# Optimization experiments

Measured on AMD Instinct MI355X. Metric: run time of the kernel, lower is better.

The kernel has to match this reference:

```python
import jax, jax.numpy as jnp
import numpy as np

B, NF, E, A = 4096, 40, 64, 32  # batch, num feature fields, embedding_size, attention_size


def setup_inputs() -> dict:
    key = jax.random.key(0)
    kx, kw, kb, kh = jax.random.split(key, 4)
    return {
        "x": jax.random.normal(kx, (B, NF, E), dtype=jnp.float32),
        "W": jax.random.normal(kw, (E, A), dtype=jnp.float32) * 0.05,  # random_normal init
        "b": jax.random.normal(kb, (A,), dtype=jnp.float32) * 0.05,
        "h": jax.random.normal(kh, (A,), dtype=jnp.float32) * 0.05,
        "p": jnp.ones((E, 1), dtype=jnp.float32),  # 'ones' initializer
    }


def reference(x, W, b, h, p):
    nf = x.shape[1]
    # pairwise (i<j) element-wise products, same ordering as the double loop
    ii, jj = np.triu_indices(nf, k=1)
    ewp = x[:, ii, :] * x[:, jj, :]                      # (B, P, E), P = nf*(nf-1)/2
    # attention MLP: relu(ewp @ W + b) . h, then exp-normalize over pairs
    a = jax.nn.relu(jnp.einsum('bpe,ea->bpa', ewp, W) + b)  # (B, P, A)
    e = jnp.exp(jnp.sum(a * h, axis=-1))                 # (B, P)  (faithful: no max-subtract)
    att = e / jnp.sum(e, axis=1, keepdims=True)          # (B, P)
    pooled = jnp.einsum('bp,bpe->be', att, ewp)          # attention-weighted sum over pairs
    return pooled @ p                                    # (B, 1)
```

## Files before the change

kernel.cpp:

```cpp
#include <hip/hip_runtime.h>

#define NFEAT 40
#define EMB   64
#define ATT   32
#define NPAIR 780
#define NTILE 49
#define XH_S  72
#define XREG  (NFEAT * XH_S)

typedef __attribute__((ext_vector_type(8))) _Float16 f16x8;
typedef __attribute__((ext_vector_type(4))) _Float16 f16x4;
typedef __attribute__((ext_vector_type(4))) float    f32x4;
typedef __attribute__((ext_vector_type(2))) unsigned u32x2;

template <int CTRL>
__device__ __forceinline__ float dpp_add_f(float v) {
  int t = __builtin_amdgcn_update_dpp(0, __float_as_int(v), CTRL, 0xF, 0xF, true);
  return v + __int_as_float(t);
}
__device__ __forceinline__ float rowsum16(float v) {
  v = dpp_add_f<0x128>(v);
  v = dpp_add_f<0x124>(v);
  v = dpp_add_f<0x122>(v);
  v = dpp_add_f<0x121>(v);
  return v;
}

__device__ __forceinline__ float xgroup_sum(float v) {
#if __has_builtin(__builtin_amdgcn_permlane16_swap) && __has_builtin(__builtin_amdgcn_permlane32_swap)
  {
    auto a = __builtin_amdgcn_permlane16_swap(__float_as_uint(v), __float_as_uint(v), false, false);
    v = __uint_as_float(a[0]) + __uint_as_float(a[1]);
    auto b = __builtin_amdgcn_permlane32_swap(__float_as_uint(v), __float_as_uint(v), false, false);
    v = __uint_as_float(b[0]) + __uint_as_float(b[1]);
  }
#else
  v += __shfl_xor(v, 16, 64);
  v += __shfl_xor(v, 32, 64);
#endif
  return v;
}

__device__ __forceinline__ int pair_off(int i) { return 39 * i - (i * (i - 1)) / 2; }

extern "C" __global__ __launch_bounds__(256)
void afm_kernel(const float* __restrict__ xg, const float* __restrict__ Wg,
                const float* __restrict__ bg, const float* __restrict__ hg,
                const float* __restrict__ pg, float* __restrict__ outg, int nbatch) {
  __shared__ __align__(16) _Float16 xh[2 * XREG];
  __shared__ unsigned prtp[25 * 32];
  __shared__ float red[4][2];

  const int tid  = threadIdx.x;
  const int lane = tid & 63, wid = tid >> 6;
  const int l15  = lane & 15, hk = lane >> 4;
  const int half = wid & 1;
  const int breg = wid >> 1;
  const int bb   = blockIdx.x * 2 + breg;
  const bool live = bb < nbatch;

  for (int p = tid; p < NTILE * 16; p += 256) {
    int i = 0, j = 0;
    if (p < NPAIR) {
      i = (int)((79.0f - sqrtf(6241.0f - 8.0f * (float)p)) * 0.5f);
      if (i < 0) i = 0;
      while (pair_off(i + 1) <= p) ++i;
      while (pair_off(i) > p) --i;
      j = i + 1 + (p - pair_off(i));
    }
    int t = p >> 4, l = p & 15;
    prtp[(t >> 1) * 32 + l * 2 + (t & 1)] =
        (unsigned)(i * 144) | ((unsigned)(j * 144) << 16);
  }

  f16x8 wf0[2], wf1[2], wf2[2];
#pragma unroll
  for (int kk = 0; kk < 2; kk++) {
    f16x8 r0, r1, r2;
#pragma unroll
    for (int t = 0; t < 8; t++) {
      int krow = kk * 32 + hk * 8 + t;
      r0[t] = (_Float16)Wg[krow * ATT + l15];
      r1[t] = (_Float16)Wg[krow * ATT + 16 + l15];
      _Float16 pv = (_Float16)pg[krow];
      r2[t] = (l15 == 0) ? pv : (_Float16)0.f;
    }
    wf0[kk] = r0; wf1[kk] = r1; wf2[kk] = r2;
  }
  const float4 b0 = *(const float4*)&bg[hk * 4];
  const float4 b1 = *(const float4*)&bg[16 + hk * 4];
  const f32x4 cb0 = {b0.x, b0.y, b0.z, b0.w};
  const f32x4 cb1 = {b1.x, b1.y, b1.z, b1.w};
  const float L2E = 1.4426950408889634f;
  float4 h0 = *(const float4*)&hg[hk * 4];
  float4 h1 = *(const float4*)&hg[16 + hk * 4];
  h0.x *= L2E; h0.y *= L2E; h0.z *= L2E; h0.w *= L2E;
  h1.x *= L2E; h1.y *= L2E; h1.z *= L2E; h1.w *= L2E;
  const f32x4 kz = {0.f, 0.f, 0.f, 0.f};

  if (live) {
    const float4* xsrc = (const float4*)(xg + (size_t)bb * (NFEAT * EMB));
    _Float16* xw = &xh[breg * XREG];
#pragma unroll
    for (int f = lane + half * 64; f < NFEAT * EMB / 4; f += 128) {
      float4 v = xsrc[f];
      int row = f >> 4, c = (f & 15) * 4;
      f16x4 h4 = {(_Float16)v.x, (_Float16)v.y, (_Float16)v.z, (_Float16)v.w};
      *(f16x4*)&xw[row * XH_S + c] = h4;
    }
  }
  __syncthreads();

  float sum_e = 0.f, sum_es = 0.f;
  const unsigned wh = (unsigned)(breg * (XREG * 2) + hk * 16);

  auto tile = [&](unsigned pij, bool full) {
    const unsigned offi = (pij & 0xFFFFu) + wh;
    const unsigned offj = (pij >> 16) + wh;
    const f16x8 xi0 = *(const f16x8*)((const char*)xh + offi);
    const f16x8 xj0 = *(const f16x8*)((const char*)xh + offj);
    const f16x8 xi1 = *(const f16x8*)((const char*)xh + offi + 64);
    const f16x8 xj1 = *(const f16x8*)((const char*)xh + offj + 64);
    f16x8 af0 = xi0 * xj0;
    f16x8 af1 = xi1 * xj1;
    f32x4 acc0 = __builtin_amdgcn_mfma_f32_16x16x32_f16(wf0[0], af0, cb0, 0, 0, 0);
    f32x4 acc1 = __builtin_amdgcn_mfma_f32_16x16x32_f16(wf1[0], af0, cb1, 0, 0, 0);
    f32x4 acc2 = __builtin_amdgcn_mfma_f32_16x16x32_f16(wf2[0], af0, kz, 0, 0, 0);
    acc0 = __builtin_amdgcn_mfma_f32_16x16x32_f16(wf0[1], af1, acc0, 0, 0, 0);
    acc1 = __builtin_amdgcn_mfma_f32_16x16x32_f16(wf1[1], af1, acc1, 0, 0, 0);
    acc2 = __builtin_amdgcn_mfma_f32_16x16x32_f16(wf2[1], af1, acc2, 0, 0, 0);
    float va = fmaf(fmaxf(acc0[0], 0.f), h0.x,
               fmaf(fmaxf(acc0[1], 0.f), h0.y,
               fmaf(fmaxf(acc0[2], 0.f), h0.z,
                    fmaxf(acc0[3], 0.f) * h0.w)));
    float vb = fmaf(fmaxf(acc1[0], 0.f), h1.x,
               fmaf(fmaxf(acc1[1], 0.f), h1.y,
               fmaf(fmaxf(acc1[2], 0.f), h1.z,
                    fmaxf(acc1[3], 0.f) * h1.w)));
    float v = xgroup_sum(va + vb);
    float e = exp2f(v);
    if (!full) e = (l15 < 12) ? e : 0.f;
    sum_e += e;
    sum_es = fmaf(e, acc2[0], sum_es);
  };

  if (live) {
    const int k0 = half ? 12 : 0;
    const int k1 = half ? 24 : 12;
#pragma unroll 4
    for (int k = k0; k < k1; ++k) {
      u32x2 pp = *(const u32x2*)&prtp[k * 32 + l15 * 2];
      tile(pp[0], true);
      tile(pp[1], true);
    }
    if (!half) tile(prtp[24 * 32 + l15 * 2], false);

    sum_e  = rowsum16(sum_e);
    sum_es = rowsum16(sum_es);
    if (lane == 0) { red[wid][0] = sum_e; red[wid][1] = sum_es; }
  }
  __syncthreads();
  if (live && lane == 0 && half == 0) {
    float Z = red[wid][0] + red[wid + 1][0];
    float S = red[wid][1] + red[wid + 1][1];
    outg[bb] = S / Z;
  }
}

extern "C" void kernel_launch(void* const* d_in, const int* in_sizes, int n_in,
                              void* d_out, int out_size, void* d_ws, size_t ws_size,
                              hipStream_t stream) {
  const float* xg = (const float*)d_in[0];
  const float* Wg = (const float*)d_in[1];
  const float* bg = (const float*)d_in[2];
  const float* hg = (const float*)d_in[3];
  const float* pg = (const float*)d_in[4];
  float* outg = (float*)d_out;
  const int Bn = in_sizes[0] / (NFEAT * EMB);
  const int nblk = (Bn + 1) / 2;
  afm_kernel<<<dim3(nblk), dim3(256), 0, stream>>>(xg, Wg, bg, hg, pg, outg, Bn);
}
```

Measured before the change: 37.55 us.

## Assign one batch row per wave and software-pipeline pair tile loop

Each wave now handles a whole batch row instead of two waves splitting one row. Blocks cover four rows, which removes the cross-wave shared-memory reduction and the second barrier, and halves the number of blocks. The pair loop is restructured to issue all LDS loads for two tiles before the MFMAs, to prefetch the next pair-index word, and to use a shallower epilogue reduction tree. The cost is twice the LDS per block, which may lower occupancy, plus a longer serial chain per wave.

```diff
diff --git a/kernel.cpp b/kernel.cpp
--- a/kernel.cpp
+++ b/kernel.cpp
@@ -47,16 +47,13 @@
 void afm_kernel(const float* __restrict__ xg, const float* __restrict__ Wg,
                 const float* __restrict__ bg, const float* __restrict__ hg,
                 const float* __restrict__ pg, float* __restrict__ outg, int nbatch) {
-  __shared__ __align__(16) _Float16 xh[2 * XREG];
+  __shared__ __align__(16) _Float16 xh[4 * XREG];
   __shared__ unsigned prtp[25 * 32];
-  __shared__ float red[4][2];
 
   const int tid  = threadIdx.x;
   const int lane = tid & 63, wid = tid >> 6;
   const int l15  = lane & 15, hk = lane >> 4;
-  const int half = wid & 1;
-  const int breg = wid >> 1;
-  const int bb   = blockIdx.x * 2 + breg;
+  const int bb   = blockIdx.x * 4 + wid;
   const bool live = bb < nbatch;
 
   for (int p = tid; p < NTILE * 16; p += 256) {
@@ -98,11 +95,11 @@
   h1.x *= L2E; h1.y *= L2E; h1.z *= L2E; h1.w *= L2E;
   const f32x4 kz = {0.f, 0.f, 0.f, 0.f};
 
+  _Float16* xw = &xh[wid * XREG];
   if (live) {
     const float4* xsrc = (const float4*)(xg + (size_t)bb * (NFEAT * EMB));
-    _Float16* xw = &xh[breg * XREG];
 #pragma unroll
-    for (int f = lane + half * 64; f < NFEAT * EMB / 4; f += 128) {
+    for (int f = lane; f < NFEAT * EMB / 4; f += 64) {
       float4 v = xsrc[f];
       int row = f >> 4, c = (f & 15) * 4;
       f16x4 h4 = {(_Float16)v.x, (_Float16)v.y, (_Float16)v.z, (_Float16)v.w};
@@ -111,60 +108,77 @@
   }
   __syncthreads();
 
+  if (!live) return;
+  const unsigned wh = (unsigned)(wid * (XREG * 2) + hk * 16);
+
   float sum_e = 0.f, sum_es = 0.f;
-  const unsigned wh = (unsigned)(breg * (XREG * 2) + hk * 16);
 
-  auto tile = [&](unsigned pij, bool full) {
-    const unsigned offi = (pij & 0xFFFFu) + wh;
-    const unsigned offj = (pij >> 16) + wh;
-    const f16x8 xi0 = *(const f16x8*)((const char*)xh + offi);
-    const f16x8 xj0 = *(const f16x8*)((const char*)xh + offj);
-    const f16x8 xi1 = *(const f16x8*)((const char*)xh + offi + 64);
-    const f16x8 xj1 = *(const f16x8*)((const char*)xh + offj + 64);
-    f16x8 af0 = xi0 * xj0;
-    f16x8 af1 = xi1 * xj1;
-    f32x4 acc0 = __builtin_amdgcn_mfma_f32_16x16x32_f16(wf0[0], af0, cb0, 0, 0, 0);
-    f32x4 acc1 = __builtin_amdgcn_mfma_f32_16x16x32_f16(wf1[0], af0, cb1, 0, 0, 0);
-    f32x4 acc2 = __builtin_amdgcn_mfma_f32_16x16x32_f16(wf2[0], af0, kz, 0, 0, 0);
-    acc0 = __builtin_amdgcn_mfma_f32_16x16x32_f16(wf0[1], af1, acc0, 0, 0, 0);
-    acc1 = __builtin_amdgcn_mfma_f32_16x16x32_f16(wf1[1], af1, acc1, 0, 0, 0);
-    acc2 = __builtin_amdgcn_mfma_f32_16x16x32_f16(wf2[1], af1, acc2, 0, 0, 0);
-    float va = fmaf(fmaxf(acc0[0], 0.f), h0.x,
-               fmaf(fmaxf(acc0[1], 0.f), h0.y,
-               fmaf(fmaxf(acc0[2], 0.f), h0.z,
-                    fmaxf(acc0[3], 0.f) * h0.w)));
-    float vb = fmaf(fmaxf(acc1[0], 0.f), h1.x,
-               fmaf(fmaxf(acc1[1], 0.f), h1.y,
-               fmaf(fmaxf(acc1[2], 0.f), h1.z,
-                    fmaxf(acc1[3], 0.f) * h1.w)));
-    float v = xgroup_sum(va + vb);
+  auto epilogue = [&](const f32x4& a0, const f32x4& a1, const f32x4& a2, bool full) {
+    float t0 = fmaf(fmaxf(a0[0], 0.f), h0.x, fmaxf(a0[1], 0.f) * h0.y);
+    float t1 = fmaf(fmaxf(a0[2], 0.f), h0.z, fmaxf(a0[3], 0.f) * h0.w);
+    float t2 = fmaf(fmaxf(a1[0], 0.f), h1.x, fmaxf(a1[1], 0.f) * h1.y);
+    float t3 = fmaf(fmaxf(a1[2], 0.f), h1.z, fmaxf(a1[3], 0.f) * h1.w);
+    float v = xgroup_sum((t0 + t1) + (t2 + t3));
     float e = exp2f(v);
     if (!full) e = (l15 < 12) ? e : 0.f;
     sum_e += e;
-    sum_es = fmaf(e, acc2[0], sum_es);
+    sum_es = fmaf(e, a2[0], sum_es);
   };
 
-  if (live) {
-    const int k0 = half ? 12 : 0;
-    const int k1 = half ? 24 : 12;
-#pragma unroll 4
-    for (int k = k0; k < k1; ++k) {
-      u32x2 pp = *(const u32x2*)&prtp[k * 32 + l15 * 2];
-      tile(pp[0], true);
-      tile(pp[1], true);
-    }
-    if (!half) tile(prtp[24 * 32 + l15 * 2], false);
+  u32x2 pp = *(const u32x2*)&prtp[l15 * 2];
+#pragma unroll 2
+  for (int k = 0; k < 24; ++k) {
+    const unsigned oiA = (pp[0] & 0xFFFFu) + wh, ojA = (pp[0] >> 16) + wh;
+    const unsigned oiB = (pp[1] & 0xFFFFu) + wh, ojB = (pp[1] >> 16) + wh;
+    const f16x8 xiA0 = *(const f16x8*)((const char*)xh + oiA);
+    const f16x8 xjA0 = *(const f16x8*)((const char*)xh + ojA);
+    const f16x8 xiA1 = *(const f16x8*)((const char*)xh + oiA + 64);
+    const f16x8 xjA1 = *(const f16x8*)((const char*)xh + ojA + 64);
+    const f16x8 xiB0 = *(const f16x8*)((const char*)xh + oiB);
+    const f16x8 xjB0 = *(const f16x8*)((const char*)xh + ojB);
+    const f16x8 xiB1 = *(const f16x8*)((const char*)xh + oiB + 64);
+    const f16x8 xjB1 = *(const f16x8*)((const char*)xh + ojB + 64);
+    if (k < 23) pp = *(const u32x2*)&prtp[(k + 1) * 32 + l15 * 2];
+    f16x8 afA0 = xiA0 * xjA0;
+    f16x8 afA1 = xiA1 * xjA1;
+    f32x4 aA0 = __builtin_amdgcn_mfma_f32_16x16x32_f16(wf0[0], afA0, cb0, 0, 0, 0);
+    f32x4 aA1 = __builtin_amdgcn_mfma_f32_16x16x32_f16(wf1[0], afA0, cb1, 0, 0, 0);
+    f32x4 aA2 = __builtin_amdgcn_mfma_f32_16x16x32_f16(wf2[0], afA0, kz, 0, 0, 0);
+    aA0 = __builtin_amdgcn_mfma_f32_16x16x32_f16(wf0[1], afA1, aA0, 0, 0, 0);
+    aA1 = __builtin_amdgcn_mfma_f32_16x16x32_f16(wf1[1], afA1, aA1, 0, 0, 0);
+    aA2 = __builtin_amdgcn_mfma_f32_16x16x32_f16(wf2[1], afA1, aA2, 0, 0, 0);
+    f16x8 afB0 = xiB0 * xjB0;
+    f16x8 afB1 = xiB1 * xjB1;
+    f32x4 aB0 = __builtin_amdgcn_mfma_f32_16x16x32_f16(wf0[0], afB0, cb0, 0, 0, 0);
+    f32x4 aB1 = __builtin_amdgcn_mfma_f32_16x16x32_f16(wf1[0], afB0, cb1, 0, 0, 0);
+    f32x4 aB2 = __builtin_amdgcn_mfma_f32_16x16x32_f16(wf2[0], afB0, kz, 0, 0, 0);
+    aB0 = __builtin_amdgcn_mfma_f32_16x16x32_f16(wf0[1], afB1, aB0, 0, 0, 0);
+    aB1 = __builtin_amdgcn_mfma_f32_16x16x32_f16(wf1[1], afB1, aB1, 0, 0, 0);
+    aB2 = __builtin_amdgcn_mfma_f32_16x16x32_f16(wf2[1], afB1, aB2, 0, 0, 0);
+    epilogue(aA0, aA1, aA2, true);
+    epilogue(aB0, aB1, aB2, true);
+  }
+  {
+    const unsigned pij = prtp[24 * 32 + l15 * 2];
+    const unsigned oi = (pij & 0xFFFFu) + wh, oj = (pij >> 16) + wh;
+    const f16x8 xi0 = *(const f16x8*)((const char*)xh + oi);
+    const f16x8 xj0 = *(const f16x8*)((const char*)xh + oj);
+    const f16x8 xi1 = *(const f16x8*)((const char*)xh + oi + 64);
+    const f16x8 xj1 = *(const f16x8*)((const char*)xh + oj + 64);
+    f16x8 af0 = xi0 * xj0;
+    f16x8 af1 = xi1 * xj1;
+    f32x4 a0 = __builtin_amdgcn_mfma_f32_16x16x32_f16(wf0[0], af0, cb0, 0, 0, 0);
+    f32x4 a1 = __builtin_amdgcn_mfma_f32_16x16x32_f16(wf1[0], af0, cb1, 0, 0, 0);
+    f32x4 a2 = __builtin_amdgcn_mfma_f32_16x16x32_f16(wf2[0], af0, kz, 0, 0, 0);
+    a0 = __builtin_amdgcn_mfma_f32_16x16x32_f16(wf0[1], af1, a0, 0, 0, 0);
+    a1 = __builtin_amdgcn_mfma_f32_16x16x32_f16(wf1[1], af1, a1, 0, 0, 0);
+    a2 = __builtin_amdgcn_mfma_f32_16x16x32_f16(wf2[1], af1, a2, 0, 0, 0);
+    epilogue(a0, a1, a2, false);
+  }
 
-    sum_e  = rowsum16(sum_e);
-    sum_es = rowsum16(sum_es);
-    if (lane == 0) { red[wid][0] = sum_e; red[wid][1] = sum_es; }
-  }
-  __syncthreads();
-  if (live && lane == 0 && half == 0) {
-    float Z = red[wid][0] + red[wid + 1][0];
-    float S = red[wid][1] + red[wid + 1][1];
-    outg[bb] = S / Z;
-  }
+  sum_e  = rowsum16(sum_e);
+  sum_es = rowsum16(sum_es);
+  if (lane == 0) outg[bb] = sum_es / sum_e;
 }
 
 extern "C" void kernel_launch(void* const* d_in, const int* in_sizes, int n_in,
@@ -177,6 +191,6 @@
   const float* pg = (const float*)d_in[4];
   float* outg = (float*)d_out;
   const int Bn = in_sizes[0] / (NFEAT * EMB);
-  const int nblk = (Bn + 1) / 2;
+  const int nblk = (Bn + 3) / 4;
   afm_kernel<<<dim3(nblk), dim3(256), 0, stream>>>(xg, Wg, bg, hg, pg, outg, Bn);
 }
```

After: 38.95 us. +3.7%, slower.

## Split weight/pair-table prep into a pre-kernel and use one wave per batch row

Applied to the files above, without the earlier changes.

A small three-block pre-kernel builds the packed fp16 MFMA weight fragments, the pair offset table and the bias/h constants into the workspace once per call. The main kernel now runs one wave per batch row with 128-thread blocks, dropping the per-block pair-table computation, the scattered W gathers, the cross-wave reduction and both __syncthreads. Each wave then handles all 780 pairs itself and reads the pair table from global/L1 with a prefetch. The costs are a second kernel launch and fewer waves in total, so each wave's serial work doubles.

```diff
diff --git a/kernel.cpp b/kernel.cpp
--- a/kernel.cpp
+++ b/kernel.cpp
@@ -8,8 +8,11 @@
 #define XH_S  72
 #define XREG  (NFEAT * XH_S)
 
+#define WS_PRT   0
+#define WS_WF    1024
+#define WS_CONST 4096
+
 typedef __attribute__((ext_vector_type(8))) _Float16 f16x8;
-typedef __attribute__((ext_vector_type(4))) _Float16 f16x4;
 typedef __attribute__((ext_vector_type(4))) float    f32x4;
 typedef __attribute__((ext_vector_type(2))) unsigned u32x2;
 
@@ -25,7 +28,6 @@
   v = dpp_add_f<0x121>(v);
   return v;
 }
-
 __device__ __forceinline__ float xgroup_sum(float v) {
 #if __has_builtin(__builtin_amdgcn_permlane16_swap) && __has_builtin(__builtin_amdgcn_permlane32_swap)
   {
@@ -40,79 +42,107 @@
 #endif
   return v;
 }
-
 __device__ __forceinline__ int pair_off(int i) { return 39 * i - (i * (i - 1)) / 2; }
 
 extern "C" __global__ __launch_bounds__(256)
-void afm_kernel(const float* __restrict__ xg, const float* __restrict__ Wg,
-                const float* __restrict__ bg, const float* __restrict__ hg,
-                const float* __restrict__ pg, float* __restrict__ outg, int nbatch) {
+void afm_pre(const float* __restrict__ Wg, const float* __restrict__ bg,
+             const float* __restrict__ hg, const float* __restrict__ pg,
+             unsigned* __restrict__ ws) {
+  __shared__ float Wl[EMB * ATT];
+  const int tid = threadIdx.x;
+  const float L2E = 1.4426950408889634f;
+
+  if (blockIdx.x == 0) {
+    for (int f = tid; f < EMB * ATT / 4; f += 256)
+      *(float4*)&Wl[f * 4] = ((const float4*)Wg)[f];
+    __syncthreads();
+    for (int o = tid; o < 1536; o += 256) {
+      int lane = o / 24, rem = o % 24, frag = rem >> 2, pi = rem & 3;
+      int kk = frag / 3, which = frag % 3;
+      int l15 = lane & 15, hk = lane >> 4;
+      unsigned out = 0;
+#pragma unroll
+      for (int s = 0; s < 2; s++) {
+        int t = pi * 2 + s;
+        int krow = kk * 32 + hk * 8 + t;
+        float v = (which == 0) ? Wl[krow * ATT + l15]
+                : (which == 1) ? Wl[krow * ATT + 16 + l15]
+                               : ((l15 == 0) ? pg[krow] : 0.f);
+        _Float16 hv = (_Float16)v;
+        unsigned short bits = __builtin_bit_cast(unsigned short, hv);
+        out |= (unsigned)bits << (16 * s);
+      }
+      ws[WS_WF + lane * 24 + rem] = out;
+    }
+  } else if (blockIdx.x == 1) {
+    for (int p = tid; p < NTILE * 16; p += 256) {
+      int i = 0, j = 0;
+      if (p < NPAIR) {
+        i = (int)((79.0f - sqrtf(6241.0f - 8.0f * (float)p)) * 0.5f);
+        if (i < 0) i = 0;
+        while (pair_off(i + 1) <= p) ++i;
+        while (pair_off(i) > p) --i;
+        j = i + 1 + (p - pair_off(i));
+      }
+      int t = p >> 4, l = p & 15;
+      ws[WS_PRT + (t >> 1) * 32 + l * 2 + (t & 1)] =
+          (unsigned)(i * 144) | ((unsigned)(j * 144) << 16);
+    }
+  } else if (blockIdx.x == 2) {
+    for (int o = tid; o < 1024; o += 256) {
+      int lane = o >> 4, r = o & 15;
+      int hk = lane >> 4, g = r >> 2, e = r & 3;
+      float v;
+      if (g == 0)      v = bg[hk * 4 + e];
+      else if (g == 1) v = bg[16 + hk * 4 + e];
+      else if (g == 2) v = hg[hk * 4 + e] * L2E;
+      else             v = hg[16 + hk * 4 + e] * L2E;
+      ((float*)ws)[WS_CONST + o] = v;
+    }
+  }
+}
+
+extern "C" __global__ __launch_bounds__(128)
+void afm_kernel(const float* __restrict__ xg, const unsigned* __restrict__ ws,
+                float* __restrict__ outg, int nbatch) {
   __shared__ __align__(16) _Float16 xh[2 * XREG];
-  __shared__ unsigned prtp[25 * 32];
-  __shared__ float red[4][2];
-
-  const int tid  = threadIdx.x;
-  const int lane = tid & 63, wid = tid >> 6;
-  const int l15  = lane & 15, hk = lane >> 4;
-  const int half = wid & 1;
-  const int breg = wid >> 1;
-  const int bb   = blockIdx.x * 2 + breg;
-  const bool live = bb < nbatch;
-
-  for (int p = tid; p < NTILE * 16; p += 256) {
-    int i = 0, j = 0;
-    if (p < NPAIR) {
-      i = (int)((79.0f - sqrtf(6241.0f - 8.0f * (float)p)) * 0.5f);
-      if (i < 0) i = 0;
-      while (pair_off(i + 1) <= p) ++i;
-      while (pair_off(i) > p) --i;
-      j = i + 1 + (p - pair_off(i));
-    }
-    int t = p >> 4, l = p & 15;
-    prtp[(t >> 1) * 32 + l * 2 + (t & 1)] =
-        (unsigned)(i * 144) | ((unsigned)(j * 144) << 16);
-  }
-
+
+  const int lane = threadIdx.x & 63, wid = threadIdx.x >> 6;
+  const int l15 = lane & 15, hk = lane >> 4;
+  const int bb = blockIdx.x * 2 + wid;
+  if (bb >= nbatch) return;
+
+  union { uint4 u; f16x8 h; } cv;
+  const uint4* wfp = (const uint4*)(ws + WS_WF + lane * 24);
   f16x8 wf0[2], wf1[2], wf2[2];
+  cv.u = wfp[0]; wf0[0] = cv.h;
+  cv.u = wfp[1]; wf1[0] = cv.h;
+  cv.u = wfp[2]; wf2[0] = cv.h;
+  cv.u = wfp[3]; wf0[1] = cv.h;
+  cv.u = wfp[4]; wf1[1] = cv.h;
+  cv.u = wfp[5]; wf2[1] = cv.h;
+  const float4* cp = (const float4*)((const float*)ws + WS_CONST + lane * 16);
+  const float4 c0 = cp[0], c1 = cp[1];
+  const float4 h0 = cp[2], h1 = cp[3];
+  const f32x4 cb0 = {c0.x, c0.y, c0.z, c0.w};
+  const f32x4 cb1 = {c1.x, c1.y, c1.z, c1.w};
+  const f32x4 kz  = {0.f, 0.f, 0.f, 0.f};
+
+  _Float16* xw = &xh[wid * XREG];
+  const float* xsrc = xg + (size_t)bb * (NFEAT * EMB);
 #pragma unroll
-  for (int kk = 0; kk < 2; kk++) {
-    f16x8 r0, r1, r2;
-#pragma unroll
-    for (int t = 0; t < 8; t++) {
-      int krow = kk * 32 + hk * 8 + t;
-      r0[t] = (_Float16)Wg[krow * ATT + l15];
-      r1[t] = (_Float16)Wg[krow * ATT + 16 + l15];
-      _Float16 pv = (_Float16)pg[krow];
-      r2[t] = (l15 == 0) ? pv : (_Float16)0.f;
-    }
-    wf0[kk] = r0; wf1[kk] = r1; wf2[kk] = r2;
-  }
-  const float4 b0 = *(const float4*)&bg[hk * 4];
-  const float4 b1 = *(const float4*)&bg[16 + hk * 4];
-  const f32x4 cb0 = {b0.x, b0.y, b0.z, b0.w};
-  const f32x4 cb1 = {b1.x, b1.y, b1.z, b1.w};
-  const float L2E = 1.4426950408889634f;
-  float4 h0 = *(const float4*)&hg[hk * 4];
-  float4 h1 = *(const float4*)&hg[16 + hk * 4];
-  h0.x *= L2E; h0.y *= L2E; h0.z *= L2E; h0.w *= L2E;
-  h1.x *= L2E; h1.y *= L2E; h1.z *= L2E; h1.w *= L2E;
-  const f32x4 kz = {0.f, 0.f, 0.f, 0.f};
-
-  if (live) {
-    const float4* xsrc = (const float4*)(xg + (size_t)bb * (NFEAT * EMB));
-    _Float16* xw = &xh[breg * XREG];
-#pragma unroll
-    for (int f = lane + half * 64; f < NFEAT * EMB / 4; f += 128) {
-      float4 v = xsrc[f];
-      int row = f >> 4, c = (f & 15) * 4;
-      f16x4 h4 = {(_Float16)v.x, (_Float16)v.y, (_Float16)v.z, (_Float16)v.w};
-      *(f16x4*)&xw[row * XH_S + c] = h4;
-    }
-  }
-  __syncthreads();
-
+  for (int it = 0; it < 5; it++) {
+    int g0 = (it * 64 + lane) * 8;
+    float4 a = *(const float4*)&xsrc[g0];
+    float4 b = *(const float4*)&xsrc[g0 + 4];
+    int row = g0 >> 6, c = g0 & 63;
+    f16x8 v = {(_Float16)a.x, (_Float16)a.y, (_Float16)a.z, (_Float16)a.w,
+               (_Float16)b.x, (_Float16)b.y, (_Float16)b.z, (_Float16)b.w};
+    *(f16x8*)&xw[row * XH_S + c] = v;
+  }
+
+  const unsigned wh = (unsigned)(wid * (XREG * 2) + hk * 16);
   float sum_e = 0.f, sum_es = 0.f;
-  const unsigned wh = (unsigned)(breg * (XREG * 2) + hk * 16);
 
   auto tile = [&](unsigned pij, bool full) {
     const unsigned offi = (pij & 0xFFFFu) + wh;
@@ -123,48 +153,36 @@
     const f16x8 xj1 = *(const f16x8*)((const char*)xh + offj + 64);
     f16x8 af0 = xi0 * xj0;
     f16x8 af1 = xi1 * xj1;
-    f32x4 acc0 = __builtin_amdgcn_mfma_f32_16x16x32_f16(wf0[0], af0, cb0, 0, 0, 0);
-    f32x4 acc1 = __builtin_amdgcn_mfma_f32_16x16x32_f16(wf1[0], af0, cb1, 0, 0, 0);
-    f32x4 acc2 = __builtin_amdgcn_mfma_f32_16x16x32_f16(wf2[0], af0, kz, 0, 0, 0);
-    acc0 = __builtin_amdgcn_mfma_f32_16x16x32_f16(wf0[1], af1, acc0, 0, 0, 0);
-    acc1 = __builtin_amdgcn_mfma_f32_16x16x32_f16(wf1[1], af1, acc1, 0, 0, 0);
-    acc2 = __builtin_amdgcn_mfma_f32_16x16x32_f16(wf2[1], af1, acc2, 0, 0, 0);
-    float va = fmaf(fmaxf(acc0[0], 0.f), h0.x,
-               fmaf(fmaxf(acc0[1], 0.f), h0.y,
-               fmaf(fmaxf(acc0[2], 0.f), h0.z,
-                    fmaxf(acc0[3], 0.f) * h0.w)));
-    float vb = fmaf(fmaxf(acc1[0], 0.f), h1.x,
-               fmaf(fmaxf(acc1[1], 0.f), h1.y,
-               fmaf(fmaxf(acc1[2], 0.f), h1.z,
-                    fmaxf(acc1[3], 0.f) * h1.w)));
-    float v = xgroup_sum(va + vb);
+    f32x4 a0 = __builtin_amdgcn_mfma_f32_16x16x32_f16(wf0[0], af0, cb0, 0, 0, 0);
+    f32x4 a1 = __builtin_amdgcn_mfma_f32_16x16x32_f16(wf1[0], af0, cb1, 0, 0, 0);
+    f32x4 a2 = __builtin_amdgcn_mfma_f32_16x16x32_f16(wf2[0], af0, kz, 0, 0, 0);
+    a0 = __builtin_amdgcn_mfma_f32_16x16x32_f16(wf0[1], af1, a0, 0, 0, 0);
+    a1 = __builtin_amdgcn_mfma_f32_16x16x32_f16(wf1[1], af1, a1, 0, 0, 0);
+    a2 = __builtin_amdgcn_mfma_f32_16x16x32_f16(wf2[1], af1, a2, 0, 0, 0);
+    float t0 = fmaf(fmaxf(a0[0], 0.f), h0.x, fmaxf(a0[1], 0.f) * h0.y);
+    float t1 = fmaf(fmaxf(a0[2], 0.f), h0.z, fmaxf(a0[3], 0.f) * h0.w);
+    float t2 = fmaf(fmaxf(a1[0], 0.f), h1.x, fmaxf(a1[1], 0.f) * h1.y);
+    float t3 = fmaf(fmaxf(a1[2], 0.f), h1.z, fmaxf(a1[3], 0.f) * h1.w);
+    float v = xgroup_sum((t0 + t1) + (t2 + t3));
     float e = exp2f(v);
     if (!full) e = (l15 < 12) ? e : 0.f;
     sum_e += e;
-    sum_es = fmaf(e, acc2[0], sum_es);
+    sum_es = fmaf(e, a2[0], sum_es);
   };
 
-  if (live) {
-    const int k0 = half ? 12 : 0;
-    const int k1 = half ? 24 : 12;
+  u32x2 pp = *(const u32x2*)(ws + WS_PRT + l15 * 2);
 #pragma unroll 4
-    for (int k = k0; k < k1; ++k) {
-      u32x2 pp = *(const u32x2*)&prtp[k * 32 + l15 * 2];
-      tile(pp[0], true);
-      tile(pp[1], true);
-    }
-    if (!half) tile(prtp[24 * 32 + l15 * 2], false);
-
-    sum_e  = rowsum16(sum_e);
-    sum_es = rowsum16(sum_es);
-    if (lane == 0) { red[wid][0] = sum_e; red[wid][1] = sum_es; }
-  }
-  __syncthreads();
-  if (live && lane == 0 && half == 0) {
-    float Z = red[wid][0] + red[wid + 1][0];
-    float S = red[wid][1] + red[wid + 1][1];
-    outg[bb] = S / Z;
-  }
+  for (int k = 0; k < 24; ++k) {
+    const unsigned pij0 = pp[0], pij1 = pp[1];
+    if (k < 23) pp = *(const u32x2*)(ws + WS_PRT + (k + 1) * 32 + l15 * 2);
+    tile(pij0, true);
+    tile(pij1, true);
+  }
+  tile(ws[WS_PRT + 24 * 32 + l15 * 2], false);
+
+  sum_e  = rowsum16(sum_e);
+  sum_es = rowsum16(sum_es);
+  if (lane == 0) outg[bb] = sum_es / sum_e;
 }
 
 extern "C" void kernel_launch(void* const* d_in, const int* in_sizes, int n_in,
@@ -176,7 +194,8 @@
   const float* hg = (const float*)d_in[3];
   const float* pg = (const float*)d_in[4];
   float* outg = (float*)d_out;
+  unsigned* ws = (unsigned*)d_ws;
   const int Bn = in_sizes[0] / (NFEAT * EMB);
-  const int nblk = (Bn + 1) / 2;
-  afm_kernel<<<dim3(nblk), dim3(256), 0, stream>>>(xg, Wg, bg, hg, pg, outg, Bn);
-}
+  afm_pre<<<dim3(3), dim3(256), 0, stream>>>(Wg, bg, hg, pg, ws);
+  afm_kernel<<<dim3((Bn + 1) / 2), dim3(128), 0, stream>>>(xg, ws, outg, Bn);
+}
```

Measured after the change: 41.38 us. 1.1x slower.

## Assign two batch rows per wave and use packed fp16 dot for relu-h

Applied to the files above, without the earlier changes.

Restructures the work split so each wave processes two full batch rows (8 per block) instead of two waves sharing one row. This removes the cross-wave shared-memory reduction and second barrier, and interleaves independent MFMA chains for latency hiding. The relu·h step becomes packed fp16 convert, max and fdot2, and staging uses pkrtz conversion. Shared memory grows fourfold, which may reduce occupancy, and the fp16 rounding of activations before the h dot adds precision loss.

```diff
diff --git a/kernel.cpp b/kernel.cpp
--- a/kernel.cpp
+++ b/kernel.cpp
@@ -9,9 +9,9 @@
 #define XREG  (NFEAT * XH_S)
 
 typedef __attribute__((ext_vector_type(8))) _Float16 f16x8;
-typedef __attribute__((ext_vector_type(4))) _Float16 f16x4;
 typedef __attribute__((ext_vector_type(4))) float    f32x4;
 typedef __attribute__((ext_vector_type(2))) unsigned u32x2;
+typedef __attribute__((ext_vector_type(2))) __fp16   h2_t;
 
 template <int CTRL>
 __device__ __forceinline__ float dpp_add_f(float v) {
@@ -25,7 +25,6 @@
   v = dpp_add_f<0x121>(v);
   return v;
 }
-
 __device__ __forceinline__ float xgroup_sum(float v) {
 #if __has_builtin(__builtin_amdgcn_permlane16_swap) && __has_builtin(__builtin_amdgcn_permlane32_swap)
   {
@@ -40,24 +39,31 @@
 #endif
   return v;
 }
-
 __device__ __forceinline__ int pair_off(int i) { return 39 * i - (i * (i - 1)) / 2; }
+
+__device__ __forceinline__ float reludot2(float s0, float s1, h2_t h2, float c) {
+  h2_t r = __builtin_amdgcn_cvt_pkrtz(s0, s1);
+  r = __builtin_elementwise_max(r, h2_t{(__fp16)0.f, (__fp16)0.f});
+#if __has_builtin(__builtin_amdgcn_fdot2)
+  return __builtin_amdgcn_fdot2(r, h2, c, false);
+#else
+  return fmaf((float)r[0], (float)h2[0], fmaf((float)r[1], (float)h2[1], c));
+#endif
+}
 
 extern "C" __global__ __launch_bounds__(256)
 void afm_kernel(const float* __restrict__ xg, const float* __restrict__ Wg,
                 const float* __restrict__ bg, const float* __restrict__ hg,
                 const float* __restrict__ pg, float* __restrict__ outg, int nbatch) {
-  __shared__ __align__(16) _Float16 xh[2 * XREG];
+  __shared__ __align__(16) _Float16 xh[8 * XREG];
   __shared__ unsigned prtp[25 * 32];
-  __shared__ float red[4][2];
 
   const int tid  = threadIdx.x;
   const int lane = tid & 63, wid = tid >> 6;
   const int l15  = lane & 15, hk = lane >> 4;
-  const int half = wid & 1;
-  const int breg = wid >> 1;
-  const int bb   = blockIdx.x * 2 + breg;
-  const bool live = bb < nbatch;
+  const int bbA  = blockIdx.x * 8 + wid * 2;
+  const int bbB  = bbA + 1;
+  const bool liveA = bbA < nbatch, liveB = bbB < nbatch;
 
   for (int p = tid; p < NTILE * 16; p += 256) {
     int i = 0, j = 0;
@@ -92,29 +98,41 @@
   const f32x4 cb0 = {b0.x, b0.y, b0.z, b0.w};
   const f32x4 cb1 = {b1.x, b1.y, b1.z, b1.w};
   const float L2E = 1.4426950408889634f;
-  float4 h0 = *(const float4*)&hg[hk * 4];
-  float4 h1 = *(const float4*)&hg[16 + hk * 4];
-  h0.x *= L2E; h0.y *= L2E; h0.z *= L2E; h0.w *= L2E;
-  h1.x *= L2E; h1.y *= L2E; h1.z *= L2E; h1.w *= L2E;
+  const float4 hv0 = *(const float4*)&hg[hk * 4];
+  const float4 hv1 = *(const float4*)&hg[16 + hk * 4];
+  const h2_t hp0 = __builtin_amdgcn_cvt_pkrtz(hv0.x * L2E, hv0.y * L2E);
+  const h2_t hp1 = __builtin_amdgcn_cvt_pkrtz(hv0.z * L2E, hv0.w * L2E);
+  const h2_t hp2 = __builtin_amdgcn_cvt_pkrtz(hv1.x * L2E, hv1.y * L2E);
+  const h2_t hp3 = __builtin_amdgcn_cvt_pkrtz(hv1.z * L2E, hv1.w * L2E);
   const f32x4 kz = {0.f, 0.f, 0.f, 0.f};
 
-  if (live) {
-    const float4* xsrc = (const float4*)(xg + (size_t)bb * (NFEAT * EMB));
-    _Float16* xw = &xh[breg * XREG];
+  auto stage = [&](int bb, int reg) {
+    _Float16* xw = &xh[reg * XREG];
+    const float* xsrc = xg + (size_t)bb * (NFEAT * EMB);
 #pragma unroll
-    for (int f = lane + half * 64; f < NFEAT * EMB / 4; f += 128) {
-      float4 v = xsrc[f];
-      int row = f >> 4, c = (f & 15) * 4;
-      f16x4 h4 = {(_Float16)v.x, (_Float16)v.y, (_Float16)v.z, (_Float16)v.w};
-      *(f16x4*)&xw[row * XH_S + c] = h4;
+    for (int it = 0; it < 5; it++) {
+      int g0 = (it * 64 + lane) * 8;
+      float4 a = *(const float4*)&xsrc[g0];
+      float4 b = *(const float4*)&xsrc[g0 + 4];
+      int row = g0 >> 6, c = g0 & 63;
+      union { h2_t v2[4]; f16x8 v8; } pk;
+      pk.v2[0] = __builtin_amdgcn_cvt_pkrtz(a.x, a.y);
+      pk.v2[1] = __builtin_amdgcn_cvt_pkrtz(a.z, a.w);
+      pk.v2[2] = __builtin_amdgcn_cvt_pkrtz(b.x, b.y);
+      pk.v2[3] = __builtin_amdgcn_cvt_pkrtz(b.z, b.w);
+      *(f16x8*)&xh[reg * XREG + row * XH_S + c] = pk.v8;
     }
-  }
+    (void)xw;
+  };
+  if (liveA) stage(bbA, wid * 2);
+  if (liveB) stage(bbB, wid * 2 + 1);
   __syncthreads();
 
-  float sum_e = 0.f, sum_es = 0.f;
-  const unsigned wh = (unsigned)(breg * (XREG * 2) + hk * 16);
-
-  auto tile = [&](unsigned pij, bool full) {
+  const unsigned whA = (unsigned)(wid * 2 * (XREG * 2) + hk * 16);
+  const unsigned whB = whA + (unsigned)(XREG * 2);
+  float seA = 0.f, sesA = 0.f, seB = 0.f, sesB = 0.f;
+
+  auto tile = [&](unsigned pij, unsigned wh) {
     const unsigned offi = (pij & 0xFFFFu) + wh;
     const unsigned offj = (pij >> 16) + wh;
     const f16x8 xi0 = *(const f16x8*)((const char*)xh + offi);
@@ -123,47 +141,52 @@
     const f16x8 xj1 = *(const f16x8*)((const char*)xh + offj + 64);
     f16x8 af0 = xi0 * xj0;
     f16x8 af1 = xi1 * xj1;
-    f32x4 acc0 = __builtin_amdgcn_mfma_f32_16x16x32_f16(wf0[0], af0, cb0, 0, 0, 0);
-    f32x4 acc1 = __builtin_amdgcn_mfma_f32_16x16x32_f16(wf1[0], af0, cb1, 0, 0, 0);
-    f32x4 acc2 = __builtin_amdgcn_mfma_f32_16x16x32_f16(wf2[0], af0, kz, 0, 0, 0);
-    acc0 = __builtin_amdgcn_mfma_f32_16x16x32_f16(wf0[1], af1, acc0, 0, 0, 0);
-    acc1 = __builtin_amdgcn_mfma_f32_16x16x32_f16(wf1[1], af1, acc1, 0, 0, 0);
-    acc2 = __builtin_amdgcn_mfma_f32_16x16x32_f16(wf2[1], af1, acc2, 0, 0, 0);
-    float va = fmaf(fmaxf(acc0[0], 0.f), h0.x,
-               fmaf(fmaxf(acc0[1], 0.f), h0.y,
-               fmaf(fmaxf(acc0[2], 0.f), h0.z,
-                    fmaxf(acc0[3], 0.f) * h0.w)));
-    float vb = fmaf(fmaxf(acc1[0], 0.f), h1.x,
-               fmaf(fmaxf(acc1[1], 0.f), h1.y,
-               fmaf(fmaxf(acc1[2], 0.f), h1.z,
-                    fmaxf(acc1[3], 0.f) * h1.w)));
-    float v = xgroup_sum(va + vb);
+    f32x4 a0 = __builtin_amdgcn_mfma_f32_16x16x32_f16(wf0[0], af0, cb0, 0, 0, 0);
+    f32x4 a1 = __builtin_amdgcn_mfma_f32_16x16x32_f16(wf1[0], af0, cb1, 0, 0, 0);
+    f32x4 a2 = __builtin_amdgcn_mfma_f32_16x16x32_f16(wf2[0], af0, kz, 0, 0, 0);
+    a0 = __builtin_amdgcn_mfma_f32_16x16x32_f16(wf0[1], af1, a0, 0, 0, 0);
+    a1 = __builtin_amdgcn_mfma_f32_16x16x32_f16(wf1[1], af1, a1, 0, 0, 0);
+    a2 = __builtin_amdgcn_mfma_f32_16x16x32_f16(wf2[1], af1, a2, 0, 0, 0);
+    float v = reludot2(a0[0], a0[1], hp0,
+              reludot2(a0[2], a0[3], hp1,
+              reludot2(a1[0], a1[1], hp2,
+              reludot2(a1[2], a1[3], hp3, 0.f))));
+    v = xgroup_sum(v);
     float e = exp2f(v);
-    if (!full) e = (l15 < 12) ? e : 0.f;
-    sum_e += e;
-    sum_es = fmaf(e, acc2[0], sum_es);
+    return make_float2(e, a2[0]);
   };
 
-  if (live) {
-    const int k0 = half ? 12 : 0;
-    const int k1 = half ? 24 : 12;
-#pragma unroll 4
-    for (int k = k0; k < k1; ++k) {
-      u32x2 pp = *(const u32x2*)&prtp[k * 32 + l15 * 2];
-      tile(pp[0], true);
-      tile(pp[1], true);
-    }
-    if (!half) tile(prtp[24 * 32 + l15 * 2], false);
-
-    sum_e  = rowsum16(sum_e);
-    sum_es = rowsum16(sum_es);
-    if (lane == 0) { red[wid][0] = sum_e; red[wid][1] = sum_es; }
-  }
-  __syncthreads();
-  if (live && lane == 0 && half == 0) {
-    float Z = red[wid][0] + red[wid + 1][0];
-    float S = red[wid][1] + red[wid + 1][1];
-    outg[bb] = S / Z;
+  u32x2 pp = *(const u32x2*)&prtp[l15 * 2];
+#pragma unroll 1
+  for (int k = 0; k < 24; ++k) {
+    const unsigned pij0 = pp[0], pij1 = pp[1];
+    if (k < 23) pp = *(const u32x2*)&prtp[(k + 1) * 32 + l15 * 2];
+    float2 rA0 = tile(pij0, whA);
+    float2 rB0 = tile(pij0, whB);
+    seA += rA0.x;  sesA = fmaf(rA0.x, rA0.y, sesA);
+    seB += rB0.x;  sesB = fmaf(rB0.x, rB0.y, sesB);
+    float2 rA1 = tile(pij1, whA);
+    float2 rB1 = tile(pij1, whB);
+    seA += rA1.x;  sesA = fmaf(rA1.x, rA1.y, sesA);
+    seB += rB1.x;  sesB = fmaf(rB1.x, rB1.y, sesB);
+  }
+  {
+    const unsigned pt = prtp[24 * 32 + l15 * 2];
+    float2 rA = tile(pt, whA);
+    float2 rB = tile(pt, whB);
+    float eA = (l15 < 12) ? rA.x : 0.f;
+    float eB = (l15 < 12) ? rB.x : 0.f;
+    seA += eA;  sesA = fmaf(eA, rA.y, sesA);
+    seB += eB;  sesB = fmaf(eB, rB.y, sesB);
+  }
+
+  seA  = rowsum16(seA);
+  sesA = rowsum16(sesA);
+  seB  = rowsum16(seB);
+  sesB = rowsum16(sesB);
+  if (lane == 0) {
+    if (liveA) outg[bbA] = sesA / seA;
+    if (liveB) outg[bbB] = sesB / seB;
   }
 }
 
@@ -177,6 +200,5 @@
   const float* pg = (const float*)d_in[4];
   float* outg = (float*)d_out;
   const int Bn = in_sizes[0] / (NFEAT * EMB);
-  const int nblk = (Bn + 1) / 2;
-  afm_kernel<<<dim3(nblk), dim3(256), 0, stream>>>(xg, Wg, bg, hg, pg, outg, Bn);
-}
+  afm_kernel<<<dim3((Bn + 7) / 8), dim3(256), 0, stream>>>(xg, Wg, bg, hg, pg, outg, Bn);
+}
```

New measurement: 37.12 us. No clear change (-1.2%).
